# Kernel tuning notes

Hardware: AMD Instinct MI355X
Metric: run time of the kernel (lower is better)

Reference implementation:

```python
import jax, jax.numpy as jnp
import numpy as np

USER_NUM = 100000
ITEM_NUM = 50000
N_NODES = USER_NUM + ITEM_NUM
EMB = 64
N_LAYERS = 3
E_HALF = 2000000  # edges per direction; total directed edges = 4M


def _make_bipartite_edges(ku, ki):
    u = jax.random.randint(ku, (E_HALF,), 0, USER_NUM)
    i = jax.random.randint(ki, (E_HALF,), 0, ITEM_NUM) + USER_NUM
    # bidirectional: user->item and item->user
    return jnp.concatenate([u, i]), jnp.concatenate([i, u])


def setup_inputs() -> dict:
    key = jax.random.key(0)
    ks = jax.random.split(key, 6)
    U = jax.random.normal(ks[0], (USER_NUM, EMB), jnp.float32)
    I = jax.random.normal(ks[1], (ITEM_NUM, EMB), jnp.float32)
    pos_src, pos_dst = _make_bipartite_edges(ks[2], ks[3])
    neg_src, neg_dst = _make_bipartite_edges(ks[4], ks[5])
    return {"U": U, "I": I, "pos_src": pos_src, "pos_dst": pos_dst,
            "neg_src": neg_src, "neg_dst": neg_dst}


def gcn_layer(x, src, dst):
    # symmetric-normalized sum aggregation (LightGCN propagation)
    ones = jnp.ones(src.shape, x.dtype)
    deg_out = jnp.maximum(jax.ops.segment_sum(ones, src, num_segments=N_NODES), 1.0)
    deg_in = jnp.maximum(jax.ops.segment_sum(ones, dst, num_segments=N_NODES), 1.0)
    h = x * (deg_out ** -0.5)[:, None]          # pre-scale by out-degree
    agg = jax.ops.segment_sum(h[src], dst, num_segments=N_NODES)  # copy_src + sum
    return agg * (deg_in ** -0.5)[:, None]      # post-scale by in-degree


def get_embedding(U, I, src, dst):
    res_u, res_i = U, I
    emb = None
    for i in range(N_LAYERS):
        x_in = jnp.concatenate([res_u, res_i], axis=0) if i == 0 else emb
        emb = gcn_layer(x_in, src, dst)
        scale = 1.0 / (i + 2)
        res_u = res_u + emb[:USER_NUM] * scale
        res_i = res_i + emb[USER_NUM:] * scale
    return res_u, res_i


def reference(U, I, pos_src, pos_dst, neg_src, neg_dst):
    res_u, res_i = get_embedding(U, I, pos_src, pos_dst)
    h = jnp.concatenate([res_u, res_i], axis=0)  # [N, D]
    pos_pred = jnp.sum(h[pos_src] * h[pos_dst], axis=-1)  # u_dot_v per edge
    neg_pred = jnp.sum(h[neg_src] * h[neg_dst], axis=-1)
    return pos_pred, neg_pred
```

## Files before the change

### kernel.cpp

```cpp
#include <hip/hip_runtime.h>
#include <hip/hip_fp16.h>

#define USER_NUM 100000
#define ITEM_NUM 50000
#define N_NODES  150000
#define EMB      64

#define NB       586
#define CAP      12288
#define PA_CHUNK 8192

static const size_t NODE_F = (size_t)N_NODES * EMB;


__global__ __launch_bounds__(256) void partition_kernel(const int* __restrict__ u_arr,
                                                        const int* __restrict__ i_arr,
                                                        int Eh,
                                                        unsigned* __restrict__ part,
                                                        int* __restrict__ gcur) {
    __shared__ int hist[NB];
    __shared__ int hbase[NB];
    int tid = threadIdx.x;
    int start = blockIdx.x * PA_CHUNK;
    int n = min(PA_CHUNK, Eh - start);
    if (n <= 0) return;
    for (int b = tid; b < NB; b += 256) hist[b] = 0;
    __syncthreads();
    for (int k = tid; k < n; k += 256) {
        int u  = u_arr[start + k];
        int it = i_arr[start + k];
        atomicAdd(&hist[it >> 8], 1);
        atomicAdd(&hist[u  >> 8], 1);
    }
    __syncthreads();
    for (int b = tid; b < NB; b += 256) {
        int h = hist[b];
        hbase[b] = h ? atomicAdd(&gcur[b], h) : 0;
        hist[b] = 0;
    }
    __syncthreads();
    for (int k = tid; k < n; k += 256) {
        int u  = u_arr[start + k];
        int it = i_arr[start + k];
        int bI = it >> 8, bU = u >> 8;
        int o1 = atomicAdd(&hist[bI], 1);
        part[(size_t)bI * CAP + hbase[bI] + o1] = ((unsigned)(it & 255) << 24) | (unsigned)u;
        int o2 = atomicAdd(&hist[bU], 1);
        part[(size_t)bU * CAP + hbase[bU] + o2] = ((unsigned)(u & 255) << 24) | (unsigned)it;
    }
}

__global__ __launch_bounds__(1024) void bscan_kernel(const int* __restrict__ gcur,
                                                     int* __restrict__ bbase) {
    __shared__ int tmp[1024];
    int tid = threadIdx.x;
    int v = (tid < NB) ? gcur[tid] : 0;
    tmp[tid] = v;
    __syncthreads();
    for (int off = 1; off < 1024; off <<= 1) {
        int t = (tid >= off) ? tmp[tid - off] : 0;
        __syncthreads();
        tmp[tid] += t;
        __syncthreads();
    }
    if (tid < NB) bbase[tid] = tmp[tid] - v;
}

__global__ __launch_bounds__(256) void buildcsr_kernel(const unsigned* __restrict__ part,
                                                       const int* __restrict__ gcur,
                                                       const int* __restrict__ bbase,
                                                       int* __restrict__ rowptr,
                                                       float* __restrict__ rs,
                                                       int* __restrict__ adj,
                                                       int E) {
    __shared__ int cnt[256];
    __shared__ int cur[256];
    __shared__ int tmp[256];
    __shared__ int adjS[CAP];
    int b = blockIdx.x;
    int tid = threadIdx.x;
    int m = min(gcur[b], CAP);
    int base = bbase[b];
    const unsigned* bp = part + (size_t)b * CAP;
    cnt[tid] = 0;
    __syncthreads();
    for (int k = tid; k < m; k += 256) atomicAdd(&cnt[bp[k] >> 24], 1);
    __syncthreads();
    int myc = cnt[tid];
    tmp[tid] = myc;
    __syncthreads();
    for (int off = 1; off < 256; off <<= 1) {
        int t = (tid >= off) ? tmp[tid - off] : 0;
        __syncthreads();
        tmp[tid] += t;
        __syncthreads();
    }
    int excl = tmp[tid] - myc;
    int node = b * 256 + tid;
    if (node < N_NODES) {
        rowptr[node] = base + excl;
        rs[node] = rsqrtf(fmaxf((float)myc, 1.0f));
    }
    if (b == 0 && tid == 0) rowptr[N_NODES] = E;
    cur[tid] = excl;
    __syncthreads();
    for (int k = tid; k < m; k += 256) {
        unsigned p = bp[k];
        int off = atomicAdd(&cur[p >> 24], 1);
        adjS[off] = (int)(p & 0xFFFFFFu);
    }
    __syncthreads();
    for (int k = tid; k < m; k += 256) adj[base + k] = adjS[k];
}


__device__ __forceinline__ unsigned int packh2(float x, float y) {
    __half2 h = __floats2half2_rn(x, y);
    return *(unsigned int*)&h;
}

__global__ __launch_bounds__(256) void init_kernel(const float* __restrict__ U,
                                                   const float* __restrict__ I,
                                                   const float* __restrict__ rs,
                                                   __half* __restrict__ xs,
                                                   float* __restrict__ res) {
    size_t i8 = (size_t)blockIdx.x * blockDim.x + threadIdx.x;
    size_t n8 = NODE_F / 8;
    if (i8 >= n8) return;
    size_t i = i8 * 8;
    const size_t ucnt = (size_t)USER_NUM * EMB;
    float4 a, b;
    if (i < ucnt) { a = *(const float4*)(U + i); b = *(const float4*)(U + i + 4); }
    else          { a = *(const float4*)(I + (i - ucnt)); b = *(const float4*)(I + (i - ucnt) + 4); }
    *(float4*)(res + i)     = a;
    *(float4*)(res + i + 4) = b;
    float r = rs[i / EMB];
    uint4 pk;
    pk.x = packh2(a.x * r, a.y * r);
    pk.y = packh2(a.z * r, a.w * r);
    pk.z = packh2(b.x * r, b.y * r);
    pk.w = packh2(b.z * r, b.w * r);
    *(uint4*)(xs + i) = pk;
}

__global__ __launch_bounds__(256) void gather_kernel(const int* __restrict__ rowptr,
                                                     const int* __restrict__ adj,
                                                     const __half* __restrict__ xs,
                                                     const float* __restrict__ rs,
                                                     float* __restrict__ res,
                                                     __half* __restrict__ xs_next,
                                                     __half* __restrict__ hout,
                                                     float scale) {
    int wv = (int)(((unsigned)blockIdx.x * 256u + threadIdx.x) >> 6);
    if (wv >= N_NODES) return;
    int lane = threadIdx.x & 63;
    int g = lane & 7;
    int d = lane >> 3;
    int beg = rowptr[wv], end = rowptr[wv + 1];
    float acc[8] = {0.f, 0.f, 0.f, 0.f, 0.f, 0.f, 0.f, 0.f};

    for (int j = beg; j < end; j += 64) {
        int nloc = min(64, end - j);
        int id = (lane < nloc) ? adj[j + lane] : 0;
        int nfull = nloc >> 3;
        for (int k = 0; k < nfull; k++) {
            int s = __shfl(id, k * 8 + g);
            uint4 raw = *(const uint4*)(xs + (size_t)s * EMB + d * 8);
            const __half2* hp = (const __half2*)&raw;
            float2 f;
            f = __half22float2(hp[0]); acc[0] += f.x; acc[1] += f.y;
            f = __half22float2(hp[1]); acc[2] += f.x; acc[3] += f.y;
            f = __half22float2(hp[2]); acc[4] += f.x; acc[5] += f.y;
            f = __half22float2(hp[3]); acc[6] += f.x; acc[7] += f.y;
        }
        int rem = nloc & 7;
        if (rem) {
            int s = __shfl(id, nfull * 8 + g);
            if (g < rem) {
                uint4 raw = *(const uint4*)(xs + (size_t)s * EMB + d * 8);
                const __half2* hp = (const __half2*)&raw;
                float2 f;
                f = __half22float2(hp[0]); acc[0] += f.x; acc[1] += f.y;
                f = __half22float2(hp[1]); acc[2] += f.x; acc[3] += f.y;
                f = __half22float2(hp[2]); acc[4] += f.x; acc[5] += f.y;
                f = __half22float2(hp[3]); acc[6] += f.x; acc[7] += f.y;
            }
        }
    }

    #pragma unroll
    for (int m = 1; m < 8; m <<= 1) {
        #pragma unroll
        for (int t = 0; t < 8; t++) acc[t] += __shfl_xor(acc[t], m);
    }

    if (g == 0) {
        float r = rs[wv];
        size_t o = (size_t)wv * EMB + d * 8;
        float4 r0 = *(float4*)(res + o);
        float4 r1 = *(float4*)(res + o + 4);
        float v0 = acc[0] * r, v1 = acc[1] * r, v2 = acc[2] * r, v3 = acc[3] * r;
        float v4 = acc[4] * r, v5 = acc[5] * r, v6 = acc[6] * r, v7 = acc[7] * r;
        r0.x += v0 * scale; r0.y += v1 * scale; r0.z += v2 * scale; r0.w += v3 * scale;
        r1.x += v4 * scale; r1.y += v5 * scale; r1.z += v6 * scale; r1.w += v7 * scale;
        *(float4*)(res + o)     = r0;
        *(float4*)(res + o + 4) = r1;
        if (xs_next) {
            uint4 pk;
            pk.x = packh2(v0 * r, v1 * r);
            pk.y = packh2(v2 * r, v3 * r);
            pk.z = packh2(v4 * r, v5 * r);
            pk.w = packh2(v6 * r, v7 * r);
            *(uint4*)(xs_next + o) = pk;
        }
        if (hout) {
            uint4 pk;
            pk.x = packh2(r0.x, r0.y);
            pk.y = packh2(r0.z, r0.w);
            pk.z = packh2(r1.x, r1.y);
            pk.w = packh2(r1.z, r1.w);
            *(uint4*)(hout + o) = pk;
        }
    }
}

__global__ __launch_bounds__(256) void dot2_kernel(const int* __restrict__ src,
                                                   const int* __restrict__ dst,
                                                   int Eh,
                                                   const __half* __restrict__ h,
                                                   float* __restrict__ out) {
    long long tid = (long long)blockIdx.x * blockDim.x + threadIdx.x;
    int e = (int)(tid >> 3);
    if (e >= Eh) return;
    int sub = (int)(tid & 7);
    int s = src[e];
    int t = dst[e];
    uint4 ra = *(const uint4*)(h + (size_t)s * EMB + sub * 8);
    uint4 rb = *(const uint4*)(h + (size_t)t * EMB + sub * 8);
    const __half2* ha = (const __half2*)&ra;
    const __half2* hb = (const __half2*)&rb;
    float dsum = 0.f;
    #pragma unroll
    for (int q = 0; q < 4; q++) {
        float2 fa = __half22float2(ha[q]);
        float2 fb = __half22float2(hb[q]);
        dsum += fa.x * fb.x + fa.y * fb.y;
    }
    dsum += __shfl_xor(dsum, 1);
    dsum += __shfl_xor(dsum, 2);
    dsum += __shfl_xor(dsum, 4);
    if (sub == 0) {
        out[e] = dsum;
        out[e + Eh] = dsum;
    }
}


extern "C" void kernel_launch(void* const* d_in, const int* in_sizes, int n_in,
                              void* d_out, int out_size, void* d_ws, size_t ws_size,
                              hipStream_t stream) {
    const float* U       = (const float*)d_in[0];
    const float* I       = (const float*)d_in[1];
    const int*   pos_src = (const int*)d_in[2];
    const int*   pos_dst = (const int*)d_in[3];
    const int*   neg_src = (const int*)d_in[4];
    const int*   neg_dst = (const int*)d_in[5];
    const int E  = in_sizes[2];
    const int Eh = E / 2;
    float* out = (float*)d_out;

    char* p = (char*)d_ws;
    auto take = [&](size_t bytes) {
        char* r = p;
        p += (bytes + 255) & ~(size_t)255;
        return r;
    };
    int*    gcur   = (int*)take((size_t)NB * 4);
    int*    bbase  = (int*)take((size_t)NB * 4);
    int*    rowptr = (int*)take(((size_t)N_NODES + 1) * 4);
    float*  rs     = (float*)take((size_t)N_NODES * 4);
    int*    adj    = (int*)take((size_t)E * 4);
    float*  res    = (float*)take(NODE_F * 4);
    __half* xsA    = (__half*)take(NODE_F * 2);
    char*   uni    = take(NODE_F * 2 * 2);
    unsigned* part = (unsigned*)uni;
    __half* xsB    = (__half*)uni;
    __half* h16    = (__half*)(uni + NODE_F * 2);

    const int B = 256;

    hipMemsetAsync(gcur, 0, (size_t)NB * 4, stream);
    partition_kernel<<<(Eh + PA_CHUNK - 1) / PA_CHUNK, B, 0, stream>>>(pos_src, pos_dst,
                                                                       Eh, part, gcur);
    bscan_kernel<<<1, 1024, 0, stream>>>(gcur, bbase);
    buildcsr_kernel<<<NB, B, 0, stream>>>(part, gcur, bbase, rowptr, rs, adj, E);

    size_t n8 = NODE_F / 8;
    init_kernel<<<(int)((n8 + B - 1) / B), B, 0, stream>>>(U, I, rs, xsA, res);

    int gblk = (N_NODES * 64 + B - 1) / B;
    gather_kernel<<<gblk, B, 0, stream>>>(rowptr, adj, xsA, rs, res, xsB, (__half*)nullptr, 1.0f / 2.0f);
    gather_kernel<<<gblk, B, 0, stream>>>(rowptr, adj, xsB, rs, res, xsA, (__half*)nullptr, 1.0f / 3.0f);
    gather_kernel<<<gblk, B, 0, stream>>>(rowptr, adj, xsA, rs, res, (__half*)nullptr, h16, 1.0f / 4.0f);

    long long nthread = (long long)Eh * 8;
    int nblk = (int)((nthread + B - 1) / B);
    dot2_kernel<<<nblk, B, 0, stream>>>(pos_src, pos_dst, Eh, h16, out);
    dot2_kernel<<<nblk, B, 0, stream>>>(neg_src, neg_dst, Eh, h16, out + E);
}
```

Measured before the change: 472.3 us.

## Keep residual embeddings in fp16 and accumulate neighbor sums in half2

The fp32 residual buffer becomes an fp16 buffer that the final gather writes and the dot kernels read directly, so the separate h16 output disappears. Neighbor accumulation and the cross-lane reduction switch from fp32 to packed half2 adds, and the dot product uses the fdot2 builtin when it is available. This cuts residual read/write traffic, converts fewer values and does fewer ALU ops in the gather loop. It loses precision and risks overflow or rounding error when summing many neighbors in fp16.

```diff
diff --git a/kernel.cpp b/kernel.cpp
--- a/kernel.cpp
+++ b/kernel.cpp
@@ -11,6 +11,8 @@
 #define PA_CHUNK 8192
 
 static const size_t NODE_F = (size_t)N_NODES * EMB;
+
+typedef _Float16 h2v __attribute__((ext_vector_type(2)));
 
 
 __global__ __launch_bounds__(256) void partition_kernel(const int* __restrict__ u_arr,
@@ -123,7 +125,7 @@
                                                    const float* __restrict__ I,
                                                    const float* __restrict__ rs,
                                                    __half* __restrict__ xs,
-                                                   float* __restrict__ res) {
+                                                   __half* __restrict__ res16) {
     size_t i8 = (size_t)blockIdx.x * blockDim.x + threadIdx.x;
     size_t n8 = NODE_F / 8;
     if (i8 >= n8) return;
@@ -132,8 +134,12 @@
     float4 a, b;
     if (i < ucnt) { a = *(const float4*)(U + i); b = *(const float4*)(U + i + 4); }
     else          { a = *(const float4*)(I + (i - ucnt)); b = *(const float4*)(I + (i - ucnt) + 4); }
-    *(float4*)(res + i)     = a;
-    *(float4*)(res + i + 4) = b;
+    uint4 pr;
+    pr.x = packh2(a.x, a.y);
+    pr.y = packh2(a.z, a.w);
+    pr.z = packh2(b.x, b.y);
+    pr.w = packh2(b.z, b.w);
+    *(uint4*)(res16 + i) = pr;
     float r = rs[i / EMB];
     uint4 pk;
     pk.x = packh2(a.x * r, a.y * r);
@@ -147,9 +153,8 @@
                                                      const int* __restrict__ adj,
                                                      const __half* __restrict__ xs,
                                                      const float* __restrict__ rs,
-                                                     float* __restrict__ res,
+                                                     __half* __restrict__ res16,
                                                      __half* __restrict__ xs_next,
-                                                     __half* __restrict__ hout,
                                                      float scale) {
     int wv = (int)(((unsigned)blockIdx.x * 256u + threadIdx.x) >> 6);
     if (wv >= N_NODES) return;
@@ -157,7 +162,9 @@
     int g = lane & 7;
     int d = lane >> 3;
     int beg = rowptr[wv], end = rowptr[wv + 1];
-    float acc[8] = {0.f, 0.f, 0.f, 0.f, 0.f, 0.f, 0.f, 0.f};
+    __half2 acch[4];
+    acch[0] = __float2half2_rn(0.f);
+    acch[1] = acch[0]; acch[2] = acch[0]; acch[3] = acch[0];
 
     for (int j = beg; j < end; j += 64) {
         int nloc = min(64, end - j);
@@ -167,11 +174,10 @@
             int s = __shfl(id, k * 8 + g);
             uint4 raw = *(const uint4*)(xs + (size_t)s * EMB + d * 8);
             const __half2* hp = (const __half2*)&raw;
-            float2 f;
-            f = __half22float2(hp[0]); acc[0] += f.x; acc[1] += f.y;
-            f = __half22float2(hp[1]); acc[2] += f.x; acc[3] += f.y;
-            f = __half22float2(hp[2]); acc[4] += f.x; acc[5] += f.y;
-            f = __half22float2(hp[3]); acc[6] += f.x; acc[7] += f.y;
+            acch[0] = __hadd2(acch[0], hp[0]);
+            acch[1] = __hadd2(acch[1], hp[1]);
+            acch[2] = __hadd2(acch[2], hp[2]);
+            acch[3] = __hadd2(acch[3], hp[3]);
         }
         int rem = nloc & 7;
         if (rem) {
@@ -179,11 +185,10 @@
             if (g < rem) {
                 uint4 raw = *(const uint4*)(xs + (size_t)s * EMB + d * 8);
                 const __half2* hp = (const __half2*)&raw;
-                float2 f;
-                f = __half22float2(hp[0]); acc[0] += f.x; acc[1] += f.y;
-                f = __half22float2(hp[1]); acc[2] += f.x; acc[3] += f.y;
-                f = __half22float2(hp[2]); acc[4] += f.x; acc[5] += f.y;
-                f = __half22float2(hp[3]); acc[6] += f.x; acc[7] += f.y;
+                acch[0] = __hadd2(acch[0], hp[0]);
+                acch[1] = __hadd2(acch[1], hp[1]);
+                acch[2] = __hadd2(acch[2], hp[2]);
+                acch[3] = __hadd2(acch[3], hp[3]);
             }
         }
     }
@@ -191,20 +196,33 @@
     #pragma unroll
     for (int m = 1; m < 8; m <<= 1) {
         #pragma unroll
-        for (int t = 0; t < 8; t++) acc[t] += __shfl_xor(acc[t], m);
+        for (int q = 0; q < 4; q++) {
+            unsigned o = __shfl_xor(*(unsigned*)&acch[q], m);
+            acch[q] = __hadd2(acch[q], *(__half2*)&o);
+        }
     }
 
     if (g == 0) {
         float r = rs[wv];
+        float2 f0 = __half22float2(acch[0]);
+        float2 f1 = __half22float2(acch[1]);
+        float2 f2 = __half22float2(acch[2]);
+        float2 f3 = __half22float2(acch[3]);
+        float v0 = f0.x * r, v1 = f0.y * r, v2 = f1.x * r, v3 = f1.y * r;
+        float v4 = f2.x * r, v5 = f2.y * r, v6 = f3.x * r, v7 = f3.y * r;
         size_t o = (size_t)wv * EMB + d * 8;
-        float4 r0 = *(float4*)(res + o);
-        float4 r1 = *(float4*)(res + o + 4);
-        float v0 = acc[0] * r, v1 = acc[1] * r, v2 = acc[2] * r, v3 = acc[3] * r;
-        float v4 = acc[4] * r, v5 = acc[5] * r, v6 = acc[6] * r, v7 = acc[7] * r;
-        r0.x += v0 * scale; r0.y += v1 * scale; r0.z += v2 * scale; r0.w += v3 * scale;
-        r1.x += v4 * scale; r1.y += v5 * scale; r1.z += v6 * scale; r1.w += v7 * scale;
-        *(float4*)(res + o)     = r0;
-        *(float4*)(res + o + 4) = r1;
+        uint4 cur = *(uint4*)(res16 + o);
+        const __half2* cp = (const __half2*)&cur;
+        float2 c0 = __half22float2(cp[0]);
+        float2 c1 = __half22float2(cp[1]);
+        float2 c2 = __half22float2(cp[2]);
+        float2 c3 = __half22float2(cp[3]);
+        uint4 nr;
+        nr.x = packh2(c0.x + v0 * scale, c0.y + v1 * scale);
+        nr.y = packh2(c1.x + v2 * scale, c1.y + v3 * scale);
+        nr.z = packh2(c2.x + v4 * scale, c2.y + v5 * scale);
+        nr.w = packh2(c3.x + v6 * scale, c3.y + v7 * scale);
+        *(uint4*)(res16 + o) = nr;
         if (xs_next) {
             uint4 pk;
             pk.x = packh2(v0 * r, v1 * r);
@@ -212,14 +230,6 @@
             pk.z = packh2(v4 * r, v5 * r);
             pk.w = packh2(v6 * r, v7 * r);
             *(uint4*)(xs_next + o) = pk;
-        }
-        if (hout) {
-            uint4 pk;
-            pk.x = packh2(r0.x, r0.y);
-            pk.y = packh2(r0.z, r0.w);
-            pk.z = packh2(r1.x, r1.y);
-            pk.w = packh2(r1.z, r1.w);
-            *(uint4*)(hout + o) = pk;
         }
     }
 }
@@ -242,9 +252,13 @@
     float dsum = 0.f;
     #pragma unroll
     for (int q = 0; q < 4; q++) {
+#if __has_builtin(__builtin_amdgcn_fdot2)
+        dsum = __builtin_amdgcn_fdot2(*(const h2v*)&ha[q], *(const h2v*)&hb[q], dsum, false);
+#else
         float2 fa = __half22float2(ha[q]);
         float2 fb = __half22float2(hb[q]);
         dsum += fa.x * fb.x + fa.y * fb.y;
+#endif
     }
     dsum += __shfl_xor(dsum, 1);
     dsum += __shfl_xor(dsum, 2);
@@ -280,12 +294,11 @@
     int*    rowptr = (int*)take(((size_t)N_NODES + 1) * 4);
     float*  rs     = (float*)take((size_t)N_NODES * 4);
     int*    adj    = (int*)take((size_t)E * 4);
-    float*  res    = (float*)take(NODE_F * 4);
     __half* xsA    = (__half*)take(NODE_F * 2);
     char*   uni    = take(NODE_F * 2 * 2);
     unsigned* part = (unsigned*)uni;
     __half* xsB    = (__half*)uni;
-    __half* h16    = (__half*)(uni + NODE_F * 2);
+    __half* res16  = (__half*)(uni + NODE_F * 2);
 
     const int B = 256;
 
@@ -296,15 +309,15 @@
     buildcsr_kernel<<<NB, B, 0, stream>>>(part, gcur, bbase, rowptr, rs, adj, E);
 
     size_t n8 = NODE_F / 8;
-    init_kernel<<<(int)((n8 + B - 1) / B), B, 0, stream>>>(U, I, rs, xsA, res);
+    init_kernel<<<(int)((n8 + B - 1) / B), B, 0, stream>>>(U, I, rs, xsA, res16);
 
     int gblk = (N_NODES * 64 + B - 1) / B;
-    gather_kernel<<<gblk, B, 0, stream>>>(rowptr, adj, xsA, rs, res, xsB, (__half*)nullptr, 1.0f / 2.0f);
-    gather_kernel<<<gblk, B, 0, stream>>>(rowptr, adj, xsB, rs, res, xsA, (__half*)nullptr, 1.0f / 3.0f);
-    gather_kernel<<<gblk, B, 0, stream>>>(rowptr, adj, xsA, rs, res, (__half*)nullptr, h16, 1.0f / 4.0f);
+    gather_kernel<<<gblk, B, 0, stream>>>(rowptr, adj, xsA, rs, res16, xsB, 1.0f / 2.0f);
+    gather_kernel<<<gblk, B, 0, stream>>>(rowptr, adj, xsB, rs, res16, xsA, 1.0f / 3.0f);
+    gather_kernel<<<gblk, B, 0, stream>>>(rowptr, adj, xsA, rs, res16, (__half*)nullptr, 1.0f / 4.0f);
 
     long long nthread = (long long)Eh * 8;
     int nblk = (int)((nthread + B - 1) / B);
-    dot2_kernel<<<nblk, B, 0, stream>>>(pos_src, pos_dst, Eh, h16, out);
-    dot2_kernel<<<nblk, B, 0, stream>>>(neg_src, neg_dst, Eh, h16, out + E);
-}
+    dot2_kernel<<<nblk, B, 0, stream>>>(pos_src, pos_dst, Eh, res16, out);
+    dot2_kernel<<<nblk, B, 0, stream>>>(neg_src, neg_dst, Eh, res16, out + E);
+}
```

After: 453.2 us. -4.0%, faster.
